# Kernel optimization log

Measured on AMD Instinct MI355X. Metric: run time of the kernel, lower is better.

## Reference

```python
import jax, jax.numpy as jnp
import numpy as np

CLIP = 10.0  # tanh clipping constant (Kool et al. C=10)


def setup_inputs() -> dict:
    key = jax.random.key(0)
    kq, kk, kv, km = jax.random.split(key, 4)
    B, M, N, D = 16, 2048, 2048, 128
    Q = jax.random.normal(kq, (B, M, D), dtype=jnp.float32)
    K = jax.random.normal(kk, (B, N, D), dtype=jnp.float32)
    V = jax.random.normal(kv, (B, N, D), dtype=jnp.float32)
    # mask: [B, N, 1] bool; True means "forbidden" (set logit to -inf).
    # p=0.3 so every row keeps plenty of valid keys (no all-masked rows).
    mask = jax.random.bernoulli(km, 0.3, (B, N, 1))
    return {"Q": Q, "K": K, "V": V, "mask": mask}


def reference(Q, K, V, mask):
    d_k = jnp.asarray(K.shape[-1], dtype=Q.dtype)
    # logits: [B, M, N]
    logits = jnp.einsum("bmd,bnd->bmn", Q, K) / jnp.sqrt(d_k)
    logits = CLIP * jnp.tanh(logits)
    # mask [B, N, 1] -> [B, 1, N], broadcast over query dim
    mask_t = jnp.transpose(mask, (0, 2, 1))
    logits = jnp.where(mask_t, -jnp.inf, logits)
    probs = jax.nn.softmax(logits, axis=-1)
    return jnp.einsum("bmn,bnd->bmd", probs, V)
```

## Files before the change

kernel.cpp:

```cpp
#include <hip/hip_runtime.h>
#include <hip/hip_fp16.h>

typedef _Float16 h8 __attribute__((ext_vector_type(8)));
typedef _Float16 h4 __attribute__((ext_vector_type(4)));
typedef float f32x4 __attribute__((ext_vector_type(4)));
typedef float f32x16 __attribute__((ext_vector_type(16)));
typedef unsigned int u32x2 __attribute__((ext_vector_type(2)));
typedef unsigned int u32x4 __attribute__((ext_vector_type(4)));

#define MFMA16(a, b, c) __builtin_amdgcn_mfma_f32_16x16x32_f16((a), (b), (c), 0, 0, 0)
#define MFMA32(a, b, c) __builtin_amdgcn_mfma_f32_32x32x16_f16((a), (b), (c), 0, 0, 0)

static constexpr int MM = 2048, NN = 2048, DD = 128;
static constexpr int NT = 16;
static constexpr size_t KV_IMG = (size_t)16 * 16 * 32768;
static constexpr size_t IND_IMG = 65536;
static constexpr size_t WS_NEED = 2 * KV_IMG + IND_IMG + 32768 * 4;

static constexpr float C1 = 0.25503487f;
static constexpr float C2 = 28.853900817779268f;
static constexpr float CVALID = 14.426950408889634f;
static constexpr float CMASK = -1.0e30f;

__device__ inline void glds16(const void* g, void* l) {
  __builtin_amdgcn_global_load_lds(
      (const __attribute__((address_space(1))) void*)g,
      (__attribute__((address_space(3))) void*)l, 16, 0, 0);
}

__global__ __launch_bounds__(256) void prep_bias(const void* __restrict__ mraw,
                                                 float* __restrict__ biasC) {
  const int tid = threadIdx.x;
  const unsigned int* mw = (const unsigned int*)mraw;
  const unsigned char* mby = (const unsigned char*)mraw;
  int okW = 1;
  for (int w = tid; w < 8192; w += 256) {
    unsigned int v = mw[w];
    okW &= (v == 0u || v == 1u || v == 0x3f800000u) ? 1 : 0;
  }
  __shared__ int sW;
  if (tid == 0) sW = 1;
  __syncthreads();
  if (!okW) atomicAnd(&sW, 0);
  __syncthreads();
  const int i = blockIdx.x * 256 + tid;
  bool masked = sW ? (mw[i] != 0u) : (mby[i] != 0);
  biasC[i] = masked ? CMASK : CVALID;
}

__global__ __launch_bounds__(256) void prep_all(
    const float* __restrict__ K, const float* __restrict__ V,
    const void* __restrict__ mraw, unsigned char* __restrict__ kimg,
    unsigned char* __restrict__ vimg, _Float16* __restrict__ ind) {
  const int id = blockIdx.x;
  const int tid = threadIdx.x;
  if (id < 512) {
    const int bt = id;
    const float* src = K + (size_t)bt * 64 * DD;
    unsigned char* dst = kimg + (size_t)(bt >> 1) * 32768 + (bt & 1) * 16384;
#pragma unroll
    for (int it = 0; it < 4; ++it) {
      const int key = (tid >> 4) + 16 * it;
      const int o = tid & 15;
      f32x4 a = *(const f32x4*)(src + key * DD + 8 * o);
      f32x4 c = *(const f32x4*)(src + key * DD + 8 * o + 4);
      h8 hv;
#pragma unroll
      for (int j = 0; j < 4; ++j) {
        hv[j] = (_Float16)(a[j] * C1);
        hv[j + 4] = (_Float16)(c[j] * C1);
      }
      *(h8*)(dst + key * 256 + ((16 * o) ^ ((key & 7) << 4))) = hv;
    }
  } else {
    const int bt = id - 512;
    const unsigned int* mw = (const unsigned int*)mraw;
    const unsigned char* mby = (const unsigned char*)mraw;
    int okW = 1;
    for (int w = tid; w < 8192; w += 256) {
      unsigned int v = mw[w];
      okW &= (v == 0u || v == 1u || v == 0x3f800000u) ? 1 : 0;
    }
    __shared__ int sW;
    __shared__ float sip[64];
    if (tid == 0) sW = 1;
    __syncthreads();
    if (!okW) atomicAnd(&sW, 0);
    __syncthreads();
    if (tid < 64) {
      const int gk = bt * 64 + tid;
      bool masked = sW ? (mw[gk] != 0u) : (mby[gk] != 0);
      sip[tid] = masked ? 0.0f : 1.0f;
      ind[gk] = masked ? (_Float16)0.0f : (_Float16)1.0f;
    }
    __syncthreads();
    const float* src = V + (size_t)bt * 64 * DD;
    unsigned char* dst = vimg + (size_t)(bt >> 1) * 32768;
    const int d = tid & 127;
    const int half = tid >> 7;
#pragma unroll
    for (int ki = 0; ki < 4; ++ki) {
      const int koct = half * 4 + ki;
      h8 w;
#pragma unroll
      for (int q = 0; q < 8; ++q)
        w[q] = (_Float16)(src[(8 * koct + q) * DD + d] * sip[8 * koct + q]);
      const int g = (bt & 1) * 8 + koct;
      *(h8*)(dst + d * 256 + ((g * 16) ^ ((d & 7) << 4))) = w;
    }
  }
}

__global__ __launch_bounds__(256, 1) void attn_main(
    const float* __restrict__ Qg, const unsigned char* __restrict__ kimg,
    const unsigned char* __restrict__ vimg, const _Float16* __restrict__ indg,
    float* __restrict__ out) {
  __shared__ __align__(16) unsigned char smem[135680];
  const int tid = threadIdx.x;
  const int lane = tid & 63;
  const int wv = tid >> 6;
  const int l31 = lane & 31;
  const int hp = lane >> 5;
  const int qg = wv >> 1;
  const int kh = wv & 1;
  const int bid = blockIdx.x;
  const int b = 2 * (bid & 7) + (bid >> 7);
  const int mt = (bid >> 3) & 15;

  const unsigned char* kib = kimg + (size_t)b * 16 * 32768;
  const unsigned char* vib = vimg + (size_t)b * 16 * 32768;
  unsigned char* sind = smem + 131072;

  h8 qa[2][8];
#pragma unroll
  for (int qgrp = 0; qgrp < 2; ++qgrp) {
    const float* qr =
        Qg + ((size_t)b * MM + mt * 128 + qg * 64 + qgrp * 32 + l31) * DD;
#pragma unroll
    for (int st = 0; st < 8; ++st) {
      const int d0 = 16 * st + 8 * hp;
      f32x4 a = *(const f32x4*)(qr + d0);
      f32x4 c = *(const f32x4*)(qr + d0 + 4);
      h8 hi;
#pragma unroll
      for (int j = 0; j < 4; ++j) {
        hi[j] = (_Float16)a[j];
        hi[j + 4] = (_Float16)c[j];
      }
      qa[qgrp][st] = hi;
    }
  }

  f32x16 oacc[2][4];
#pragma unroll
  for (int qgrp = 0; qgrp < 2; ++qgrp)
#pragma unroll
    for (int dc = 0; dc < 4; ++dc)
#pragma unroll
      for (int j = 0; j < 16; ++j) oacc[qgrp][dc][j] = 0.f;
  f32x16 rsacc[2];
#pragma unroll
  for (int qgrp = 0; qgrp < 2; ++qgrp)
#pragma unroll
    for (int j = 0; j < 16; ++j) rsacc[qgrp][j] = 0.f;

  auto stage = [&](int tn, int bi) {
    const unsigned char* kt = kib + (size_t)tn * 32768;
    const unsigned char* vt = vib + (size_t)tn * 32768;
    unsigned char* dst = smem + bi * 65536;
#pragma unroll
    for (int i = 0; i < 8; ++i) {
      const int off = wv * 8192 + i * 1024;
      glds16(kt + off + lane * 16, dst + off);
      glds16(vt + off + lane * 16, dst + 32768 + off);
    }
  };

  glds16((const unsigned char*)indg + (size_t)b * 4096 + wv * 1024 + lane * 16,
         sind + wv * 1024);
  stage(0, 0);
  __syncthreads();

  const int ksw = (l31 & 7) << 4;

  for (int tn = 0; tn < NT; ++tn) {
    const unsigned char* kbuf = smem + (tn & 1) * 65536;
    const unsigned char* vbuf = kbuf + 32768;
    if (tn + 1 < NT) stage(tn + 1, (tn + 1) & 1);

#pragma unroll
    for (int kg = 0; kg < 2; ++kg) {
      const int key = 64 * kh + 32 * kg + l31;
      const int krow = key << 8;

      f32x16 s[2];
#pragma unroll
      for (int j = 0; j < 16; ++j) { s[0][j] = 0.f; s[1][j] = 0.f; }
#pragma unroll
      for (int st = 0; st < 8; ++st) {
        h8 kf = *(const h8*)(kbuf + krow + ((32 * st + 16 * hp) ^ ksw));
        s[0] = MFMA32(kf, qa[0][st], s[0]);
        s[1] = MFMA32(kf, qa[1][st], s[1]);
      }

      h8 pb[2][2];
#pragma unroll
      for (int qgrp = 0; qgrp < 2; ++qgrp) {
        unsigned pkA[4], pkB[4];
#pragma unroll
        for (int jq = 0; jq < 4; ++jq) {
          float p[4];
#pragma unroll
          for (int i = 0; i < 4; ++i) {
            const float u = __builtin_amdgcn_exp2f(s[qgrp][4 * jq + i]);
            p[i] = __builtin_amdgcn_exp2f(
                fmaf(-C2, __builtin_amdgcn_rcpf(u + 1.0f), CVALID));
          }
          pkA[jq] = __builtin_bit_cast(unsigned,
                                       __builtin_amdgcn_cvt_pkrtz(p[0], p[1]));
          pkB[jq] = __builtin_bit_cast(unsigned,
                                       __builtin_amdgcn_cvt_pkrtz(p[2], p[3]));
        }
#pragma unroll
        for (int ks = 0; ks < 2; ++ks) {
          u32x2 sa = __builtin_amdgcn_permlane32_swap(
              pkA[2 * ks], pkA[2 * ks + 1], false, false);
          u32x2 sb = __builtin_amdgcn_permlane32_swap(
              pkB[2 * ks], pkB[2 * ks + 1], false, false);
          u32x4 w = {sa[0], sb[0], sa[1], sb[1]};
          pb[qgrp][ks] = __builtin_bit_cast(h8, w);
        }
      }

#pragma unroll
      for (int ks = 0; ks < 2; ++ks) {
        h8 ia = *(const h8*)(sind + tn * 256 + 128 * kh + 64 * kg + 32 * ks +
                             16 * hp);
        rsacc[0] = MFMA32(ia, pb[0][ks], rsacc[0]);
        rsacc[1] = MFMA32(ia, pb[1][ks], rsacc[1]);
      }

#pragma unroll
      for (int dc = 0; dc < 4; ++dc) {
        const int vrow = (32 * dc + l31) << 8;
#pragma unroll
        for (int ks = 0; ks < 2; ++ks) {
          h8 vf = *(const h8*)(vbuf + vrow +
                               ((128 * kh + 64 * kg + 32 * ks + 16 * hp) ^
                                ksw));
          oacc[0][dc] = MFMA32(vf, pb[0][ks], oacc[0][dc]);
          oacc[1][dc] = MFMA32(vf, pb[1][ks], oacc[1][dc]);
        }
      }
    }
    __syncthreads();
  }

  float* olds = (float*)smem;
  float* rs1 = (float*)(smem + 135168);
  if (kh == 1) {
#pragma unroll
    for (int qgrp = 0; qgrp < 2; ++qgrp) {
      const int row = qg * 64 + qgrp * 32 + l31;
#pragma unroll
      for (int dc = 0; dc < 4; ++dc)
#pragma unroll
        for (int jq = 0; jq < 4; ++jq) {
          f32x4 v = {oacc[qgrp][dc][4 * jq + 0], oacc[qgrp][dc][4 * jq + 1],
                     oacc[qgrp][dc][4 * jq + 2], oacc[qgrp][dc][4 * jq + 3]};
          *(f32x4*)&olds[row * 132 + 32 * dc + 8 * jq + 4 * hp] = v;
        }
      if (hp == 0) rs1[row] = rsacc[qgrp][0];
    }
  }
  __syncthreads();
  if (kh == 0) {
#pragma unroll
    for (int qgrp = 0; qgrp < 2; ++qgrp) {
      const int row = qg * 64 + qgrp * 32 + l31;
      const float inv = __builtin_amdgcn_rcpf(rsacc[qgrp][0] + rs1[row]);
#pragma unroll
      for (int dc = 0; dc < 4; ++dc)
#pragma unroll
        for (int jq = 0; jq < 4; ++jq) {
          float* pp = &olds[row * 132 + 32 * dc + 8 * jq + 4 * hp];
          f32x4 v = *(const f32x4*)pp;
          v[0] = (v[0] + oacc[qgrp][dc][4 * jq + 0]) * inv;
          v[1] = (v[1] + oacc[qgrp][dc][4 * jq + 1]) * inv;
          v[2] = (v[2] + oacc[qgrp][dc][4 * jq + 2]) * inv;
          v[3] = (v[3] + oacc[qgrp][dc][4 * jq + 3]) * inv;
          *(f32x4*)pp = v;
        }
    }
  }
  __syncthreads();
  float* ob = out + ((size_t)b * MM + mt * 128) * DD;
#pragma unroll
  for (int c = 0; c < 16; ++c) {
    const int idx = c * 1024 + tid * 4;
    const int r2 = idx >> 7, col = idx & 127;
    *(f32x4*)&ob[r2 * 128 + col] = *(const f32x4*)&olds[r2 * 132 + col];
  }
}

__global__ __launch_bounds__(256, 2) void attn_fallback(
    const float* __restrict__ Qg, const float* __restrict__ Kg,
    const float* __restrict__ Vg, const float* __restrict__ biasC,
    float* __restrict__ out) {
  __shared__ __align__(16) unsigned char smem[51456];
  const int tid = threadIdx.x;
  const int lane = tid & 63;
  const int wv = tid >> 6;
  const int r = lane & 15;
  const int g = lane >> 4;
  const int rw = wv >> 1;
  const int h = wv & 1;
  const int b = blockIdx.x >> 5;
  const int mt = blockIdx.x & 31;
  const int m0 = mt * 64 + rw * 32;

  float* blds = (float*)(smem + 43264);
  {
    const float* cb = biasC + b * NN;
#pragma unroll
    for (int i = 0; i < 8; ++i) blds[tid + 256 * i] = cb[tid + 256 * i];
  }
  h8 qh[2][4];
  {
    const float* qb = Qg + ((size_t)b * MM + m0) * DD;
#pragma unroll
    for (int rf = 0; rf < 2; ++rf) {
      const float* qr = qb + (16 * rf + r) * DD;
#pragma unroll
      for (int t = 0; t < 4; ++t) {
        f32x4 a = *(const f32x4*)(qr + 32 * t + 8 * g);
        f32x4 c = *(const f32x4*)(qr + 32 * t + 8 * g + 4);
        h8 hi;
#pragma unroll
        for (int j = 0; j < 4; ++j) {
          hi[j] = (_Float16)a[j];
          hi[j + 4] = (_Float16)c[j];
        }
        qh[rf][t] = hi;
      }
    }
  }
  f32x4 acc[2][8];
#pragma unroll
  for (int rf = 0; rf < 2; ++rf)
#pragma unroll
    for (int cd = 0; cd < 8; ++cd) acc[rf][cd] = (f32x4){0.f, 0.f, 0.f, 0.f};
  float rs[2][4] = {{0.f, 0.f, 0.f, 0.f}, {0.f, 0.f, 0.f, 0.f}};
  const float* kb = Kg + (size_t)b * NN * DD;
  const float* vbp = Vg + (size_t)b * NN * DD;
  _Float16* plds = (_Float16*)(smem + 32768 + wv * 2560);
  const int bk0 = tid >> 5, bd0 = tid & 31;
  const int bk1 = (256 + tid) >> 5, bd1 = tid & 31;
  f32x4 kpre[8], vpre[8];
#pragma unroll
  for (int i = 0; i < 8; ++i) kpre[i] = *(const f32x4*)(kb + i * 1024 + tid * 4);
#pragma unroll
  for (int q = 0; q < 4; ++q) {
    vpre[q] = *(const f32x4*)(vbp + (4 * bk0 + q) * DD + 4 * bd0);
    vpre[4 + q] = *(const f32x4*)(vbp + (4 * bk1 + q) * DD + 4 * bd1);
  }
  for (int tn = 0; tn < 32; ++tn) {
#pragma unroll
    for (int i = 0; i < 8; ++i) {
      const int flat = i * 1024 + tid * 4;
      const int kkey = flat >> 7;
      const int d0 = flat & 127;
      h4 hv;
#pragma unroll
      for (int j = 0; j < 4; ++j) hv[j] = (_Float16)kpre[i][j];
      *(h4*)(smem + (kkey << 8) + ((d0 << 1) ^ ((kkey & 7) << 4))) = hv;
    }
#pragma unroll
    for (int it = 0; it < 2; ++it) {
      const int bk = it ? bk1 : bk0;
      const int bd = it ? bd1 : bd0;
#pragma unroll
      for (int p = 0; p < 4; ++p) {
        h4 w;
#pragma unroll
        for (int q = 0; q < 4; ++q) w[q] = (_Float16)vpre[it * 4 + q][p];
        const int d = 4 * bd + p;
        *(h4*)(smem + 16384 + (d << 7) +
               ((bk << 3) ^ (((d >> 1) & 7) << 4))) = w;
      }
    }
    if (tn + 1 < 32) {
      const float* ks = kb + (tn + 1) * 64 * DD;
      const float* vs = vbp + (tn + 1) * 64 * DD;
#pragma unroll
      for (int i = 0; i < 8; ++i) kpre[i] = *(const f32x4*)(ks + i * 1024 + tid * 4);
#pragma unroll
      for (int q = 0; q < 4; ++q) {
        vpre[q] = *(const f32x4*)(vs + (4 * bk0 + q) * DD + 4 * bd0);
        vpre[4 + q] = *(const f32x4*)(vs + (4 * bk1 + q) * DD + 4 * bd1);
      }
    }
    __syncthreads();
#pragma unroll
    for (int c = 0; c < 2; ++c) {
      f32x4 S0 = {0.f, 0.f, 0.f, 0.f}, S1 = {0.f, 0.f, 0.f, 0.f};
      const int kkey = h * 32 + 16 * c + r;
      const int krow = kkey << 8;
      const int ksw = (kkey & 7) << 4;
#pragma unroll
      for (int t = 0; t < 4; ++t) {
        h8 kf = *(const h8*)(smem + krow + ((64 * t + 16 * g) ^ ksw));
        S0 = MFMA16(qh[0][t], kf, S0);
        S1 = MFMA16(qh[1][t], kf, S1);
      }
      const float Cc = blds[tn * 64 + kkey];
#pragma unroll
      for (int j = 0; j < 4; ++j) {
        float u0 = __builtin_amdgcn_exp2f(S0[j] * C1);
        float p0 = __builtin_amdgcn_exp2f(
            fmaf(-C2, __builtin_amdgcn_rcpf(u0 + 1.0f), Cc));
        rs[0][j] += p0;
        plds[(4 * g + j) * 40 + 16 * c + r] = (_Float16)p0;
        float u1 = __builtin_amdgcn_exp2f(S1[j] * C1);
        float p1 = __builtin_amdgcn_exp2f(
            fmaf(-C2, __builtin_amdgcn_rcpf(u1 + 1.0f), Cc));
        rs[1][j] += p1;
        plds[(16 + 4 * g + j) * 40 + 16 * c + r] = (_Float16)p1;
      }
    }
    h8 a0 = *(const h8*)((unsigned char*)plds + r * 80 + 16 * g);
    h8 a1 = *(const h8*)((unsigned char*)plds + (16 + r) * 80 + 16 * g);
#pragma unroll
    for (int cd = 0; cd < 8; ++cd) {
      const int d = 16 * cd + r;
      h8 vf = *(const h8*)(smem + 16384 + (d << 7) +
                           ((64 * h + 16 * g) ^ (((d >> 1) & 7) << 4)));
      acc[0][cd] = MFMA16(a0, vf, acc[0][cd]);
      acc[1][cd] = MFMA16(a1, vf, acc[1][cd]);
    }
    __syncthreads();
  }
#pragma unroll
  for (int rf = 0; rf < 2; ++rf)
#pragma unroll
    for (int j = 0; j < 4; ++j) {
      float v = rs[rf][j];
      v += __shfl_xor(v, 1);
      v += __shfl_xor(v, 2);
      v += __shfl_xor(v, 4);
      v += __shfl_xor(v, 8);
      rs[rf][j] = v;
    }
  float* olds = (float*)smem;
  float* rslds = (float*)(smem + 43008);
  if (h == 1) {
    float* my = olds + rw * 4096;
#pragma unroll
    for (int rf = 0; rf < 2; ++rf)
#pragma unroll
      for (int cd = 0; cd < 8; ++cd)
#pragma unroll
        for (int j = 0; j < 4; ++j)
          my[(16 * rf + 4 * g + j) * 128 + 16 * cd + r] = acc[rf][cd][j];
    if (r == 0) {
#pragma unroll
      for (int rf = 0; rf < 2; ++rf)
#pragma unroll
        for (int j = 0; j < 4; ++j)
          rslds[rw * 32 + 16 * rf + 4 * g + j] = rs[rf][j];
    }
  }
  __syncthreads();
  if (h == 0) {
    const float* ot = olds + rw * 4096;
    float* ob = out + ((size_t)b * MM + m0) * DD;
#pragma unroll
    for (int rf = 0; rf < 2; ++rf)
#pragma unroll
      for (int j = 0; j < 4; ++j) {
        const int rl = 16 * rf + 4 * g + j;
        const float tot = rs[rf][j] + rslds[rw * 32 + rl];
        const float inv = __builtin_amdgcn_rcpf(tot);
#pragma unroll
        for (int cd = 0; cd < 8; ++cd) {
          float v = acc[rf][cd][j] + ot[rl * 128 + 16 * cd + r];
          ob[rl * DD + 16 * cd + r] = v * inv;
        }
      }
  }
}

extern "C" void kernel_launch(void* const* d_in, const int* in_sizes, int n_in,
                              void* d_out, int out_size, void* d_ws, size_t ws_size,
                              hipStream_t stream) {
  const float* Q = (const float*)d_in[0];
  const float* K = (const float*)d_in[1];
  const float* V = (const float*)d_in[2];
  const void* mask = d_in[3];
  float* out = (float*)d_out;
  if (ws_size >= WS_NEED) {
    unsigned char* kimg = (unsigned char*)d_ws;
    unsigned char* vimg = kimg + KV_IMG;
    _Float16* ind = (_Float16*)(vimg + KV_IMG);
    prep_all<<<dim3(1024), dim3(256), 0, stream>>>(K, V, mask, kimg, vimg, ind);
    attn_main<<<dim3(256), dim3(256), 0, stream>>>(Q, kimg, vimg, ind, out);
  } else {
    float* biasC = (float*)d_ws;
    prep_bias<<<dim3(128), dim3(256), 0, stream>>>(mask, biasC);
    attn_fallback<<<dim3(512), dim3(256), 0, stream>>>(Q, K, V, biasC, out);
  }
}
```

Before: 78.50 us.

## Split key tile across four waves per query group with 512-thread blocks

Doubles the block to 512 threads (8 waves), so each query group's 128-key tile is split across four waves of 32 keys each instead of two waves of 64. Each wave does half the per-tile MFMA work, which raises wave-level parallelism per CU and helps hide the exp/rcp latency. MFMA sections are wrapped in s_setprio. The epilogue now reduces four partial accumulators through two swizzled LDS buffers plus per-wave row sums, and normalisation moves into the final store loop. In exchange there are more LDS reduction steps, more register pressure from the launch bound, and smem use rises slightly.

```diff
diff --git a/kernel.cpp b/kernel.cpp
--- a/kernel.cpp
+++ b/kernel.cpp
@@ -111,31 +111,27 @@
   }
 }
 
-__global__ __launch_bounds__(256, 1) void attn_main(
+__global__ __launch_bounds__(512, 2) void attn_main(
     const float* __restrict__ Qg, const unsigned char* __restrict__ kimg,
     const unsigned char* __restrict__ vimg, const _Float16* __restrict__ indg,
     float* __restrict__ out) {
-  __shared__ __align__(16) unsigned char smem[135680];
+  __shared__ __align__(16) unsigned char smem[137216];
   const int tid = threadIdx.x;
   const int lane = tid & 63;
   const int wv = tid >> 6;
   const int l31 = lane & 31;
   const int hp = lane >> 5;
-  const int qg = wv >> 1;
-  const int kh = wv & 1;
+  const int qg = wv >> 2;
+  const int kh = wv & 3;
   const int bid = blockIdx.x;
   const int b = 2 * (bid & 7) + (bid >> 7);
   const int mt = (bid >> 3) & 15;
-
-  const unsigned char* kib = kimg + (size_t)b * 16 * 32768;
-  const unsigned char* vib = vimg + (size_t)b * 16 * 32768;
-  unsigned char* sind = smem + 131072;
+  const int m0 = mt * 128 + qg * 64;
 
   h8 qa[2][8];
 #pragma unroll
   for (int qgrp = 0; qgrp < 2; ++qgrp) {
-    const float* qr =
-        Qg + ((size_t)b * MM + mt * 128 + qg * 64 + qgrp * 32 + l31) * DD;
+    const float* qr = Qg + ((size_t)b * MM + m0 + qgrp * 32 + l31) * DD;
 #pragma unroll
     for (int st = 0; st < 8; ++st) {
       const int d0 = 16 * st + 8 * hp;
@@ -164,101 +160,114 @@
 #pragma unroll
     for (int j = 0; j < 16; ++j) rsacc[qgrp][j] = 0.f;
 
-  auto stage = [&](int tn, int bi) {
-    const unsigned char* kt = kib + (size_t)tn * 32768;
-    const unsigned char* vt = vib + (size_t)tn * 32768;
-    unsigned char* dst = smem + bi * 65536;
-#pragma unroll
-    for (int i = 0; i < 8; ++i) {
-      const int off = wv * 8192 + i * 1024;
-      glds16(kt + off + lane * 16, dst + off);
-      glds16(vt + off + lane * 16, dst + 32768 + off);
-    }
-  };
-
-  glds16((const unsigned char*)indg + (size_t)b * 4096 + wv * 1024 + lane * 16,
-         sind + wv * 1024);
-  stage(0, 0);
+  const unsigned char* kib = kimg + (size_t)b * 16 * 32768;
+  const unsigned char* vib = vimg + (size_t)b * 16 * 32768;
+  unsigned char* sind = smem + 131072;
+
+#pragma unroll
+  for (int i = 0; i < 4; ++i) {
+    const int off = wv * 4096 + i * 1024;
+    glds16(kib + off + lane * 16, smem + off);
+    glds16(vib + off + lane * 16, smem + 32768 + off);
+  }
+  if (wv < 4)
+    glds16((const unsigned char*)indg + (size_t)b * 4096 + wv * 1024 + lane * 16,
+           sind + wv * 1024);
   __syncthreads();
 
   const int ksw = (l31 & 7) << 4;
+  const int krow = (32 * kh + l31) << 8;
 
   for (int tn = 0; tn < NT; ++tn) {
     const unsigned char* kbuf = smem + (tn & 1) * 65536;
     const unsigned char* vbuf = kbuf + 32768;
-    if (tn + 1 < NT) stage(tn + 1, (tn + 1) & 1);
-
-#pragma unroll
-    for (int kg = 0; kg < 2; ++kg) {
-      const int key = 64 * kh + 32 * kg + l31;
-      const int krow = key << 8;
-
-      f32x16 s[2];
-#pragma unroll
-      for (int j = 0; j < 16; ++j) { s[0][j] = 0.f; s[1][j] = 0.f; }
-#pragma unroll
-      for (int st = 0; st < 8; ++st) {
-        h8 kf = *(const h8*)(kbuf + krow + ((32 * st + 16 * hp) ^ ksw));
-        s[0] = MFMA32(kf, qa[0][st], s[0]);
-        s[1] = MFMA32(kf, qa[1][st], s[1]);
-      }
-
-      h8 pb[2][2];
-#pragma unroll
-      for (int qgrp = 0; qgrp < 2; ++qgrp) {
-        unsigned pkA[4], pkB[4];
-#pragma unroll
-        for (int jq = 0; jq < 4; ++jq) {
-          float p[4];
-#pragma unroll
-          for (int i = 0; i < 4; ++i) {
-            const float u = __builtin_amdgcn_exp2f(s[qgrp][4 * jq + i]);
-            p[i] = __builtin_amdgcn_exp2f(
-                fmaf(-C2, __builtin_amdgcn_rcpf(u + 1.0f), CVALID));
-          }
-          pkA[jq] = __builtin_bit_cast(unsigned,
-                                       __builtin_amdgcn_cvt_pkrtz(p[0], p[1]));
-          pkB[jq] = __builtin_bit_cast(unsigned,
-                                       __builtin_amdgcn_cvt_pkrtz(p[2], p[3]));
+    if (tn + 1 < NT) {
+      unsigned char* nbuf = smem + ((tn + 1) & 1) * 65536;
+      const unsigned char* ks = kib + (size_t)(tn + 1) * 32768;
+      const unsigned char* vs = vib + (size_t)(tn + 1) * 32768;
+#pragma unroll
+      for (int i = 0; i < 4; ++i) {
+        const int off = wv * 4096 + i * 1024;
+        glds16(ks + off + lane * 16, nbuf + off);
+        glds16(vs + off + lane * 16, nbuf + 32768 + off);
+      }
+    }
+
+    f32x16 s[2];
+#pragma unroll
+    for (int j = 0; j < 16; ++j) { s[0][j] = 0.f; s[1][j] = 0.f; }
+    __builtin_amdgcn_s_setprio(1);
+#pragma unroll
+    for (int st = 0; st < 8; ++st) {
+      h8 kf = *(const h8*)(kbuf + krow + ((32 * st + 16 * hp) ^ ksw));
+      s[0] = MFMA32(kf, qa[0][st], s[0]);
+      s[1] = MFMA32(kf, qa[1][st], s[1]);
+    }
+    __builtin_amdgcn_s_setprio(0);
+
+    h8 pb[2][2];
+#pragma unroll
+    for (int qgrp = 0; qgrp < 2; ++qgrp) {
+      unsigned pkA[4], pkB[4];
+#pragma unroll
+      for (int jq = 0; jq < 4; ++jq) {
+        float p[4];
+#pragma unroll
+        for (int i = 0; i < 4; ++i) {
+          const float u = __builtin_amdgcn_exp2f(s[qgrp][4 * jq + i]);
+          p[i] = __builtin_amdgcn_exp2f(
+              fmaf(-C2, __builtin_amdgcn_rcpf(u + 1.0f), CVALID));
         }
-#pragma unroll
-        for (int ks = 0; ks < 2; ++ks) {
-          u32x2 sa = __builtin_amdgcn_permlane32_swap(
-              pkA[2 * ks], pkA[2 * ks + 1], false, false);
-          u32x2 sb = __builtin_amdgcn_permlane32_swap(
-              pkB[2 * ks], pkB[2 * ks + 1], false, false);
-          u32x4 w = {sa[0], sb[0], sa[1], sb[1]};
-          pb[qgrp][ks] = __builtin_bit_cast(h8, w);
-        }
-      }
-
+        pkA[jq] = __builtin_bit_cast(unsigned,
+                                     __builtin_amdgcn_cvt_pkrtz(p[0], p[1]));
+        pkB[jq] = __builtin_bit_cast(unsigned,
+                                     __builtin_amdgcn_cvt_pkrtz(p[2], p[3]));
+      }
 #pragma unroll
       for (int ks = 0; ks < 2; ++ks) {
-        h8 ia = *(const h8*)(sind + tn * 256 + 128 * kh + 64 * kg + 32 * ks +
-                             16 * hp);
-        rsacc[0] = MFMA32(ia, pb[0][ks], rsacc[0]);
-        rsacc[1] = MFMA32(ia, pb[1][ks], rsacc[1]);
-      }
-
-#pragma unroll
-      for (int dc = 0; dc < 4; ++dc) {
-        const int vrow = (32 * dc + l31) << 8;
-#pragma unroll
-        for (int ks = 0; ks < 2; ++ks) {
-          h8 vf = *(const h8*)(vbuf + vrow +
-                               ((128 * kh + 64 * kg + 32 * ks + 16 * hp) ^
-                                ksw));
-          oacc[0][dc] = MFMA32(vf, pb[0][ks], oacc[0][dc]);
-          oacc[1][dc] = MFMA32(vf, pb[1][ks], oacc[1][dc]);
-        }
-      }
-    }
+        u32x2 sa = __builtin_amdgcn_permlane32_swap(pkA[2 * ks],
+                                                    pkA[2 * ks + 1], false,
+                                                    false);
+        u32x2 sb = __builtin_amdgcn_permlane32_swap(pkB[2 * ks],
+                                                    pkB[2 * ks + 1], false,
+                                                    false);
+        u32x4 w = {sa[0], sb[0], sa[1], sb[1]};
+        pb[qgrp][ks] = __builtin_bit_cast(h8, w);
+      }
+    }
+
+    __builtin_amdgcn_s_setprio(1);
+#pragma unroll
+    for (int ks = 0; ks < 2; ++ks) {
+      h8 ia = *(const h8*)(sind + tn * 256 + 64 * kh + 32 * ks + 16 * hp);
+      rsacc[0] = MFMA32(ia, pb[0][ks], rsacc[0]);
+      rsacc[1] = MFMA32(ia, pb[1][ks], rsacc[1]);
+    }
+#pragma unroll
+    for (int dc = 0; dc < 4; ++dc) {
+      const int vrow = (32 * dc + l31) << 8;
+#pragma unroll
+      for (int ks = 0; ks < 2; ++ks) {
+        h8 vf = *(const h8*)(vbuf + vrow +
+                             ((64 * kh + 32 * ks + 16 * hp) ^ ksw));
+        oacc[0][dc] = MFMA32(vf, pb[0][ks], oacc[0][dc]);
+        oacc[1][dc] = MFMA32(vf, pb[1][ks], oacc[1][dc]);
+      }
+    }
+    __builtin_amdgcn_s_setprio(0);
     __syncthreads();
   }
 
-  float* olds = (float*)smem;
-  float* rs1 = (float*)(smem + 135168);
-  if (kh == 1) {
+  unsigned char* bufA = smem;
+  unsigned char* bufB = smem + 65536;
+  float* rsH = (float*)(smem + 135168);
+#pragma unroll
+  for (int qgrp = 0; qgrp < 2; ++qgrp) {
+    const int row = qg * 64 + qgrp * 32 + l31;
+    if (hp == 0) rsH[kh * 128 + row] = rsacc[qgrp][0];
+  }
+  if (kh == 1 || kh == 3) {
+    unsigned char* buf = (kh == 1) ? bufA : bufB;
 #pragma unroll
     for (int qgrp = 0; qgrp < 2; ++qgrp) {
       const int row = qg * 64 + qgrp * 32 + l31;
@@ -268,27 +277,28 @@
         for (int jq = 0; jq < 4; ++jq) {
           f32x4 v = {oacc[qgrp][dc][4 * jq + 0], oacc[qgrp][dc][4 * jq + 1],
                      oacc[qgrp][dc][4 * jq + 2], oacc[qgrp][dc][4 * jq + 3]};
-          *(f32x4*)&olds[row * 132 + 32 * dc + 8 * jq + 4 * hp] = v;
+          const int dbyte = (32 * dc + 8 * jq + 4 * hp) * 4;
+          *(f32x4*)(buf + row * 512 + (dbyte ^ ((row & 31) << 4))) = v;
         }
-      if (hp == 0) rs1[row] = rsacc[qgrp][0];
     }
   }
   __syncthreads();
-  if (kh == 0) {
+  if (kh == 0 || kh == 2) {
+    unsigned char* buf = (kh == 0) ? bufA : bufB;
 #pragma unroll
     for (int qgrp = 0; qgrp < 2; ++qgrp) {
       const int row = qg * 64 + qgrp * 32 + l31;
-      const float inv = __builtin_amdgcn_rcpf(rsacc[qgrp][0] + rs1[row]);
 #pragma unroll
       for (int dc = 0; dc < 4; ++dc)
 #pragma unroll
         for (int jq = 0; jq < 4; ++jq) {
-          float* pp = &olds[row * 132 + 32 * dc + 8 * jq + 4 * hp];
+          const int dbyte = (32 * dc + 8 * jq + 4 * hp) * 4;
+          float* pp = (float*)(buf + row * 512 + (dbyte ^ ((row & 31) << 4)));
           f32x4 v = *(const f32x4*)pp;
-          v[0] = (v[0] + oacc[qgrp][dc][4 * jq + 0]) * inv;
-          v[1] = (v[1] + oacc[qgrp][dc][4 * jq + 1]) * inv;
-          v[2] = (v[2] + oacc[qgrp][dc][4 * jq + 2]) * inv;
-          v[3] = (v[3] + oacc[qgrp][dc][4 * jq + 3]) * inv;
+          v[0] += oacc[qgrp][dc][4 * jq + 0];
+          v[1] += oacc[qgrp][dc][4 * jq + 1];
+          v[2] += oacc[qgrp][dc][4 * jq + 2];
+          v[3] += oacc[qgrp][dc][4 * jq + 3];
           *(f32x4*)pp = v;
         }
     }
@@ -296,10 +306,19 @@
   __syncthreads();
   float* ob = out + ((size_t)b * MM + mt * 128) * DD;
 #pragma unroll
-  for (int c = 0; c < 16; ++c) {
-    const int idx = c * 1024 + tid * 4;
-    const int r2 = idx >> 7, col = idx & 127;
-    *(f32x4*)&ob[r2 * 128 + col] = *(const f32x4*)&olds[r2 * 132 + col];
+  for (int it = 0; it < 8; ++it) {
+    const int byte = it * 8192 + tid * 16;
+    const int r2 = byte >> 9;
+    const int g16 = byte & 511;
+    const int off = r2 * 512 + (g16 ^ ((r2 & 31) << 4));
+    f32x4 a = *(const f32x4*)(bufA + off);
+    f32x4 c = *(const f32x4*)(bufB + off);
+    const float tot =
+        rsH[r2] + rsH[128 + r2] + rsH[256 + r2] + rsH[384 + r2];
+    const float inv = __builtin_amdgcn_rcpf(tot);
+    f32x4 v = {(a[0] + c[0]) * inv, (a[1] + c[1]) * inv, (a[2] + c[2]) * inv,
+               (a[3] + c[3]) * inv};
+    *(f32x4*)((unsigned char*)ob + byte) = v;
   }
 }
 
@@ -503,7 +522,7 @@
     unsigned char* vimg = kimg + KV_IMG;
     _Float16* ind = (_Float16*)(vimg + KV_IMG);
     prep_all<<<dim3(1024), dim3(256), 0, stream>>>(K, V, mask, kimg, vimg, ind);
-    attn_main<<<dim3(256), dim3(256), 0, stream>>>(Q, kimg, vimg, ind, out);
+    attn_main<<<dim3(256), dim3(512), 0, stream>>>(Q, kimg, vimg, ind, out);
   } else {
     float* biasC = (float*)d_ws;
     prep_bias<<<dim3(128), dim3(256), 0, stream>>>(mask, biasC);
```

Result: slower. 105.0 us (+33.8%).
